# Kernel tuning notes

Hardware: AMD Instinct MI355X
Metric: run time of the kernel (lower is better)

## Reference

```python
import jax, jax.numpy as jnp
import numpy as np

TEMPERATURE = 2.0
ALPHA = 0.5
BETA = 0.5
EMB_SCALE = 0.02  # keep exp(scores) finite (original uses exp without max-subtraction)

N_TOKENS = 4096
VOCAB = 32000
DIM = 1024


def setup_inputs() -> dict:
    key = jax.random.key(0)
    k1, k2, k3, k4, k5 = jax.random.split(key, 5)
    batch = jax.random.randint(k1, (N_TOKENS,), 0, VOCAB)
    lang_emb = jax.random.normal(k2, (VOCAB, DIM), dtype=jnp.float32) * EMB_SCALE
    key_emb = jax.random.normal(k3, (VOCAB, DIM), dtype=jnp.float32) * EMB_SCALE
    value_emb = jax.random.normal(k4, (VOCAB, DIM), dtype=jnp.float32) * EMB_SCALE
    W = jax.random.normal(k5, (DIM, DIM), dtype=jnp.float32) * (1.0 / np.sqrt(DIM))
    b = jnp.zeros((DIM,), dtype=jnp.float32)
    return {"batch": batch, "lang_emb": lang_emb, "key_emb": key_emb,
            "value_emb": value_emb, "W": W, "b": b}


def reference(batch, lang_emb, key_emb, value_emb, W, b):
    # query: language-specific embedding lookup  [N, d]
    query = lang_emb[batch]
    # bilinear-transformed universal keys  [V, d]
    tkeys = key_emb @ W.T + b
    # scores = mm(tkeys, query^T).T  -> [N, V]
    scores = query @ tkeys.T
    # exp-normalize WITHOUT max subtraction, with temperature (as in original)
    w = jnp.exp(scores) / TEMPERATURE
    w = w / jnp.sum(w, axis=1, keepdims=True)
    # weighted universal value sum  [N, d]
    value = w @ value_emb
    # interpolate with direct value-embedding lookup
    return ALPHA * value_emb[batch] + BETA * value
```

## Files before the change

### kernel.cpp

```cpp
#include <hip/hip_runtime.h>


#define DIM   1024
#define VOCAB 32000
#define NTOK  4096

typedef unsigned short u16;
typedef unsigned char  u8;
typedef long long      i64t;
typedef __attribute__((ext_vector_type(2))) long long i64x2;
typedef __attribute__((ext_vector_type(8))) __bf16 bf16x8;
typedef __attribute__((ext_vector_type(4))) float  f32x4;
typedef __attribute__((ext_vector_type(8))) u16    u16x8;
typedef __attribute__((ext_vector_type(4))) u16    u16x4;
typedef __attribute__((ext_vector_type(8))) u8     u8x8;

__device__ __forceinline__ u16 f2bf(float f) {
  unsigned u = __float_as_uint(f);
  u += 0x7FFFu + ((u >> 16) & 1u);
  return (u16)(u >> 16);
}
__device__ __forceinline__ float bf2f(u16 s) {
  return __uint_as_float(((unsigned)s) << 16);
}
__device__ __forceinline__ u8 f2e4m3(float f) {
  unsigned u = __float_as_uint(f);
  unsigned s = (u >> 24) & 0x80u;
  int e = (int)((u >> 23) & 0xFF);
  unsigned m = u & 0x7FFFFF;
  int te = e - 127 + 7;
  if (te >= 1) {
    unsigned keep = m >> 20;
    unsigned rest = m & 0xFFFFF;
    keep += (rest > 0x80000u) || (rest == 0x80000u && (keep & 1));
    if (keep == 8) { keep = 0; te += 1; }
    return (u8)(s | ((unsigned)te << 3) | keep);
  } else {
    float q = fabsf(f) * 512.0f;
    int qi = (int)rintf(q);
    if (qi > 7) return (u8)(s | (1u << 3));
    return (u8)(s | (unsigned)qi);
  }
}
__device__ __forceinline__ u8 f2e4m3_exp(float e) {
  float sc = (e >= 1.0f) ? 8.0f : 16.0f;
  int   bo = (e >= 1.0f) ? 48 : 40;
  return (u8)(bo + (int)rintf(e * sc));
}
__device__ __forceinline__ int kperm(int k) {
  return ((k >> 3) & 3) * 16 + ((k >> 5) << 3) + (k & 7);
}

#define SB() __builtin_amdgcn_sched_barrier(0)
#define BAR() { SB(); __builtin_amdgcn_s_barrier(); SB(); }


__global__ void cvt_f32_bf16(const float* __restrict__ in, u16* __restrict__ out) {
  size_t i = (size_t)blockIdx.x * 256 + threadIdx.x;
  float4 v = ((const float4*)in)[i];
  u16x4 o; o[0]=f2bf(v.x); o[1]=f2bf(v.y); o[2]=f2bf(v.z); o[3]=f2bf(v.w);
  ((u16x4*)out)[i] = o;
}

__global__ void gather_q(const int* __restrict__ batch, const float* __restrict__ lang,
                         u16* __restrict__ q) {
  int row = blockIdx.x;
  int src = batch[row];
  int t = threadIdx.x;
  float4 v = *(const float4*)(lang + (size_t)src * DIM + (t << 2));
  u16x4 o; o[0]=f2bf(v.x); o[1]=f2bf(v.y); o[2]=f2bf(v.z); o[3]=f2bf(v.w);
  *(u16x4*)(q + (size_t)row * DIM + (t << 2)) = o;
}

__global__ void transpose_cvt(const float* __restrict__ in, u16* __restrict__ out,
                              int ldin, int ldout) {
  __shared__ u16 t[64][66];
  int r0 = blockIdx.x << 6;
  int c0 = blockIdx.y << 6;
  int tid = threadIdx.x;
  #pragma unroll
  for (int p = 0; p < 4; ++p) {
    int r = (p << 4) + (tid >> 4);
    int c = (tid & 15) << 2;
    float4 v = *(const float4*)(in + (size_t)(r0 + r) * ldin + c0 + c);
    t[c+0][r] = f2bf(v.x);
    t[c+1][r] = f2bf(v.y);
    t[c+2][r] = f2bf(v.z);
    t[c+3][r] = f2bf(v.w);
  }
  __syncthreads();
  #pragma unroll
  for (int qq = 0; qq < 2; ++qq) {
    int rr = tid >> 2;
    int cc = (((tid & 3) << 1) + qq) << 3;
    u16x8 w;
    #pragma unroll
    for (int j = 0; j < 8; ++j) w[j] = t[rr][cc + j];
    *(u16x8*)(out + (size_t)(c0 + rr) * ldout + r0 + cc) = w;
  }
}

__global__ void cvt_key_f8(const float* __restrict__ in, u8* __restrict__ out) {
  size_t g = (size_t)blockIdx.x * 256 + threadIdx.x;
  size_t row = g >> 7;
  int gg = (int)(g & 127);
  int b = gg >> 3, G = gg & 7;
  int O = ((G & 1) << 2) + (G >> 1);
  const float* src = in + row * DIM + (b << 6) + (O << 3);
  float4 v0 = *(const float4*)src;
  float4 v1 = *(const float4*)(src + 4);
  u8x8 o;
  o[0]=f2e4m3(16.f*v0.x); o[1]=f2e4m3(16.f*v0.y); o[2]=f2e4m3(16.f*v0.z); o[3]=f2e4m3(16.f*v0.w);
  o[4]=f2e4m3(16.f*v1.x); o[5]=f2e4m3(16.f*v1.y); o[6]=f2e4m3(16.f*v1.z); o[7]=f2e4m3(16.f*v1.w);
  *(u8x8*)(out + row * DIM + (b << 6) + (G << 3)) = o;
}

__global__ void cvt_qw_f8(const u16* __restrict__ in, u8* __restrict__ out) {
  size_t g = (size_t)blockIdx.x * 256 + threadIdx.x;
  size_t row = g >> 7;
  int gg = (int)(g & 127);
  int b = gg >> 3, G = gg & 7;
  int O = ((G & 1) << 2) + (G >> 1);
  u16x8 v = *(const u16x8*)(in + row * DIM + (b << 6) + (O << 3));
  u8x8 o;
  #pragma unroll
  for (int j = 0; j < 8; ++j) o[j] = f2e4m3(16.f * bf2f(v[j]));
  *(u8x8*)(out + row * DIM + (b << 6) + (G << 3)) = o;
}

__global__ void transpose_cvt_f8(const float* __restrict__ in, u8* __restrict__ out) {
  __shared__ float t[64][65];
  int r0 = blockIdx.x << 6;
  int c0 = blockIdx.y << 6;
  int tid = threadIdx.x;
  #pragma unroll
  for (int p = 0; p < 4; ++p) {
    int r = (p << 4) + (tid >> 4);
    int c = (tid & 15) << 2;
    float4 v = *(const float4*)(in + (size_t)(r0 + r) * DIM + c0 + c);
    t[c+0][r] = v.x; t[c+1][r] = v.y; t[c+2][r] = v.z; t[c+3][r] = v.w;
  }
  __syncthreads();
  #pragma unroll
  for (int qq = 0; qq < 2; ++qq) {
    int rr = tid >> 2;
    int O  = ((tid & 3) << 1) + qq;
    int cc = O << 3;
    int Gp = ((O & 3) << 1) + (O >> 2);
    u8x8 w;
    #pragma unroll
    for (int j = 0; j < 8; ++j) w[j] = f2e4m3(16.f * t[rr][cc + j]);
    *(u8x8*)(out + (size_t)(c0 + rr) * VOCAB + r0 + (Gp << 3)) = w;
  }
}

__global__ void gemm_qw(const u16* __restrict__ A, const u16* __restrict__ B,
                        u16* __restrict__ C, int K, int kSteps, int ldc) {
  __shared__ u16 As[128 * 32];
  __shared__ u16 Bs[128 * 32];
  const int tid  = threadIdx.x;
  const int lane = tid & 63;
  const int wid  = tid >> 6;
  const int wr   = wid >> 1, wc = wid & 1;
  const int row0 = blockIdx.x << 7;
  const int col0 = blockIdx.y << 7;

  f32x4 acc[4][4];
  #pragma unroll
  for (int m = 0; m < 4; ++m)
    #pragma unroll
    for (int n = 0; n < 4; ++n) acc[m][n] = (f32x4){0.f,0.f,0.f,0.f};

  const int sr = lane >> 2;
  const int sc = (lane & 3) << 3;

  for (int ks = 0; ks < kSteps; ++ks) {
    const int kk = ks << 5;
    #pragma unroll
    for (int t = 0; t < 2; ++t) {
      const int i = wid * 2 + t;
      const u16* gA = A + (size_t)(row0 + (i << 4) + sr) * K + kk + sc;
      const u16* gB = B + (size_t)(col0 + (i << 4) + sr) * K + kk + sc;
      __builtin_amdgcn_global_load_lds((const __attribute__((address_space(1))) void*)gA,
                                       (__attribute__((address_space(3))) void*)(As + i * 512),
                                       16, 0, 0);
      __builtin_amdgcn_global_load_lds((const __attribute__((address_space(1))) void*)gB,
                                       (__attribute__((address_space(3))) void*)(Bs + i * 512),
                                       16, 0, 0);
    }
    __syncthreads();
    bf16x8 a[4], b[4];
    #pragma unroll
    for (int m = 0; m < 4; ++m)
      a[m] = *(const bf16x8*)(As + ((wr << 6) + (m << 4) + (lane & 15)) * 32 + ((lane >> 4) << 3));
    #pragma unroll
    for (int n = 0; n < 4; ++n)
      b[n] = *(const bf16x8*)(Bs + ((wc << 6) + (n << 4) + (lane & 15)) * 32 + ((lane >> 4) << 3));
    #pragma unroll
    for (int m = 0; m < 4; ++m)
      #pragma unroll
      for (int n = 0; n < 4; ++n)
        acc[m][n] = __builtin_amdgcn_mfma_f32_16x16x32_bf16(a[m], b[n], acc[m][n], 0, 0, 0);
    __syncthreads();
  }

  const int r0 = row0 + (wr << 6);
  const int c0 = col0 + (wc << 6);
  const int fq = (lane >> 4) << 2;
  const int fr = lane & 15;
  #pragma unroll
  for (int m = 0; m < 4; ++m)
    #pragma unroll
    for (int n = 0; n < 4; ++n) {
      int col = c0 + (n << 4) + fr;
      #pragma unroll
      for (int j = 0; j < 4; ++j) {
        int row = r0 + (m << 4) + fq + j;
        C[(size_t)row * ldc + col] = f2bf(acc[m][n][j]);
      }
    }
}

#define STG8E(s, kk)                                                               \
  {                                                                                \
    _Pragma("unroll")                                                              \
    for (int c = 0; c < 4; ++c) {                                                  \
      const int ra = (c << 6) + (tid >> 3);                                        \
      const int ua = (tid & 7) ^ ((ra >> 1) & 7);                                  \
      const u8* gA = A + (size_t)(row0 + ra) * Kb + (kk) + (ua << 4);              \
      __builtin_amdgcn_global_load_lds(                                            \
          (const __attribute__((address_space(1))) void*)gA,                       \
          (__attribute__((address_space(3))) void*)(lds + (s) * 65536 + (c << 13) + tid * 16), \
          16, 0, 0);                                                               \
    }                                                                              \
    _Pragma("unroll")                                                              \
    for (int c = 0; c < 4; ++c) {                                                  \
      const int rn = (c << 6) + (tid >> 3);                                        \
      const int un = (tid & 7) ^ ((rn >> 1) & 7);                                  \
      const u8* gB = B + (size_t)(col0 + rn) * Kb + (kk) + (un << 4);              \
      __builtin_amdgcn_global_load_lds(                                            \
          (const __attribute__((address_space(1))) void*)gB,                       \
          (__attribute__((address_space(3))) void*)(lds + (s) * 65536 + 32768 + (c << 13) + tid * 16), \
          16, 0, 0);                                                               \
    }                                                                              \
  }

#define KTILE128(t, NT)                                                            \
  {                                                                                \
    SB(); asm volatile("s_waitcnt vmcnt(0)"); SB();                                \
    BAR();                                                                         \
    if ((t) + 1 < (NT)) STG8E(((t) + 1) & 1, (((t) + 1) << 7) + kb0)               \
    const u8* Ab = lds + ((t) & 1) * 65536;                                        \
    const u8* Bb = Ab + 32768;                                                     \
    _Pragma("unroll")                                                              \
    for (int nh = 0; nh < 2; ++nh)                                                 \
      _Pragma("unroll")                                                            \
      for (int nq = 0; nq < 2; ++nq) {                                             \
        const int row = (wc << 6) + (nh << 5) + (nq << 4) + fr;                    \
        const int sw  = (row >> 1) & 7;                                            \
        i64x2 v0 = *(const i64x2*)(Bb + row * 128 + ((fq ^ sw) << 4));             \
        b0[nh][nq][0] = v0[0]; b0[nh][nq][1] = v0[1];                              \
        i64x2 v1 = *(const i64x2*)(Bb + row * 128 + (((4 + fq) ^ sw) << 4));       \
        b1[nh][nq][0] = v1[0]; b1[nh][nq][1] = v1[1];                              \
      }                                                                            \
    _Pragma("unroll")                                                              \
    for (int mq = 0; mq < 8; ++mq) {                                               \
      const int row = (wr << 7) + ((mq >> 2) << 6) + ((mq & 3) << 4) + fr;         \
      const int sw  = (row >> 1) & 7;                                              \
      i64x2 v0 = *(const i64x2*)(Ab + row * 128 + ((fq ^ sw) << 4));               \
      a0[mq][0] = v0[0]; a0[mq][1] = v0[1];                                        \
      i64x2 v1 = *(const i64x2*)(Ab + row * 128 + (((4 + fq) ^ sw) << 4));         \
      a1[mq][0] = v1[0]; a1[mq][1] = v1[1];                                        \
    }                                                                              \
    __builtin_amdgcn_s_setprio(1);                                                 \
    _Pragma("unroll")                                                              \
    for (int m = 0; m < 8; ++m)                                                    \
      _Pragma("unroll")                                                            \
      for (int nh = 0; nh < 2; ++nh)                                               \
        _Pragma("unroll")                                                          \
        for (int nq = 0; nq < 2; ++nq)                                             \
          _Pragma("unroll")                                                        \
          for (int ks = 0; ks < 2; ++ks)                                           \
            acc[m][(nh << 1) + nq] = __builtin_amdgcn_mfma_f32_16x16x32_fp8_fp8(   \
                a0[m][ks], b0[nh][nq][ks], acc[m][(nh << 1) + nq], 0, 0, 0);       \
    _Pragma("unroll")                                                              \
    for (int m = 0; m < 8; ++m)                                                    \
      _Pragma("unroll")                                                            \
      for (int nh = 0; nh < 2; ++nh)                                               \
        _Pragma("unroll")                                                          \
        for (int nq = 0; nq < 2; ++nq)                                             \
          _Pragma("unroll")                                                        \
          for (int ks = 0; ks < 2; ++ks)                                           \
            acc[m][(nh << 1) + nq] = __builtin_amdgcn_mfma_f32_16x16x32_fp8_fp8(   \
                a1[m][ks], b1[nh][nq][ks], acc[m][(nh << 1) + nq], 0, 0, 0);       \
    __builtin_amdgcn_s_setprio(0);                                                 \
  }

__global__ __launch_bounds__(512, 1) void gemm256e8(const u8* __restrict__ A,
                                                    const u8* __restrict__ B,
                                                    u8* __restrict__ P,
                                                    float* __restrict__ dpart,
                                                    int Kb, int nTiles) {
  __shared__ __align__(16) u8 lds[131072];
  const int tid  = threadIdx.x;
  const int lane = tid & 63;
  const int wid  = tid >> 6;
  const int wr   = wid >> 2;
  const int wc   = wid & 3;

  const int nwg = (int)(gridDim.x * gridDim.y);
  int lin = blockIdx.y * gridDim.x + blockIdx.x;
  { const int cpx = nwg >> 3; lin = (lin & 7) * cpx + (lin >> 3); }
  const int row0 = (lin & 15) << 8;
  const int cblk = lin >> 4;
  const int col0 = cblk << 8;
  const int kb0 = 0;

  const int fr = lane & 15;
  const int fq = lane >> 4;

  f32x4 acc[8][4];
  #pragma unroll
  for (int m = 0; m < 8; ++m)
    #pragma unroll
    for (int n = 0; n < 4; ++n) acc[m][n] = (f32x4){0.f, 0.f, 0.f, 0.f};

  i64t a0[8][2], a1[8][2], b0[2][2][2], b1[2][2][2];

  STG8E(0, kb0)
  for (int t = 0; t < nTiles; ++t) KTILE128(t, nTiles)

  const float inv256 = 1.0f / 256.0f;
  float rs[32];
  #pragma unroll
  for (int i = 0; i < 32; ++i) rs[i] = 0.f;
  #pragma unroll
  for (int m = 0; m < 8; ++m)
    #pragma unroll
    for (int n = 0; n < 4; ++n) {
      const int l6  = (n << 4) + fr;
      const int col = col0 + (wc << 6) + kperm(l6);
      #pragma unroll
      for (int j = 0; j < 4; ++j) {
        const int row = row0 + (wr << 7) + (m << 4) + (fq << 2) + j;
        float e = __expf(acc[m][n][j] * inv256);
        P[(size_t)row * VOCAB + col] = f2e4m3_exp(e);
        rs[(m << 2) + j] += e;
      }
    }
  #pragma unroll
  for (int i = 0; i < 32; ++i) {
    #pragma unroll
    for (int s = 8; s >= 1; s >>= 1) rs[i] += __shfl_xor(rs[i], s, 16);
  }
  __syncthreads();
  float* dsm = (float*)lds;
  if (fr == 0) {
    #pragma unroll
    for (int m = 0; m < 8; ++m)
      #pragma unroll
      for (int j = 0; j < 4; ++j)
        dsm[(wc << 8) + (wr << 7) + (m << 4) + (fq << 2) + j] = rs[(m << 2) + j];
  }
  __syncthreads();
  if (tid < 256)
    dpart[(size_t)(row0 + tid) * 256 + cblk] =
        dsm[tid] + dsm[256 + tid] + dsm[512 + tid] + dsm[768 + tid];
}

__global__ __launch_bounds__(512, 1) void gemm256p8(const u8* __restrict__ A,
                                                    const u8* __restrict__ B,
                                                    float* __restrict__ Cout,
                                                    int Kb) {
  __shared__ __align__(16) u8 lds[131072];
  const int tid  = threadIdx.x;
  const int lane = tid & 63;
  const int wid  = tid >> 6;
  const int wr   = wid >> 2;
  const int wc   = wid & 3;

  const int nwg = (int)(gridDim.x * gridDim.y);
  int lin = blockIdx.y * gridDim.x + blockIdx.x;
  { const int cpx = nwg >> 3; lin = (lin & 7) * cpx + (lin >> 3); }
  const int row0 = (lin & 15) << 8;
  const int col0 = (lin >> 4) << 8;

  const int z = blockIdx.z;
  const int nT = (z < 2) ? 32 : 31;
  const int kb0 = ((z < 2) ? (z * 32) : (64 + (z - 2) * 31)) << 7;

  const int fr = lane & 15;
  const int fq = lane >> 4;

  f32x4 acc[8][4];
  #pragma unroll
  for (int m = 0; m < 8; ++m)
    #pragma unroll
    for (int n = 0; n < 4; ++n) acc[m][n] = (f32x4){0.f, 0.f, 0.f, 0.f};

  i64t a0[8][2], a1[8][2], b0[2][2][2], b1[2][2][2];

  STG8E(0, kb0)
  for (int t = 0; t < nT; ++t) KTILE128(t, nT)

  float* C = Cout + (size_t)z * NTOK * DIM;
  #pragma unroll
  for (int m = 0; m < 8; ++m)
    #pragma unroll
    for (int n = 0; n < 4; ++n) {
      const int col = col0 + (wc << 6) + (n << 4) + fr;
      #pragma unroll
      for (int j = 0; j < 4; ++j) {
        const int row = row0 + (wr << 7) + (m << 4) + (fq << 2) + j;
        C[(size_t)row * DIM + col] = acc[m][n][j];
      }
    }
}

__global__ __launch_bounds__(256, 2) void gemm128e(const u16* __restrict__ A,
                                                   const u16* __restrict__ B,
                                                   u16* __restrict__ P,
                                                   float* __restrict__ dpart,
                                                   int K, int nTiles, int ldc, int cb0) {
  __shared__ __align__(16) u16 lds[32768];
  const int tid  = threadIdx.x;
  const int lane = tid & 63;
  const int wid  = tid >> 6;
  const int wr   = wid >> 1;
  const int wc   = wid & 1;

  const int nwg = (int)(gridDim.x * gridDim.y);
  int lin = blockIdx.y * gridDim.x + blockIdx.x;
  { const int cpx = nwg >> 3; lin = (lin & 7) * cpx + (lin >> 3); }
  const int row0 = (lin & 31) << 7;
  const int cblk = lin >> 5;
  const int col0 = cblk << 7;

  const int fr = lane & 15;
  const int fq = lane >> 4;
  const int rb = tid >> 3;
  const int ss = tid & 7;

#define STG128(d, kk)                                                              \
  {                                                                                \
    _Pragma("unroll")                                                              \
    for (int c = 0; c < 4; ++c) {                                                  \
      const int ra = (c << 5) + rb;                                                \
      const u16* gA = A + (size_t)(row0 + ra) * K + (kk) + ((ss ^ (ra & 7)) << 3); \
      __builtin_amdgcn_global_load_lds(                                            \
          (const __attribute__((address_space(1))) void*)gA,                       \
          (__attribute__((address_space(3))) void*)(lds + (d) * 16384 + (((c << 5) + (wid << 3)) << 6)), \
          16, 0, 0);                                                               \
    }                                                                              \
    _Pragma("unroll")                                                              \
    for (int c = 0; c < 4; ++c) {                                                  \
      const int rn = (c << 5) + rb;                                                \
      const u16* gB = B + (size_t)(col0 + rn) * K + (kk) + ((ss ^ (rn & 7)) << 3); \
      __builtin_amdgcn_global_load_lds(                                            \
          (const __attribute__((address_space(1))) void*)gB,                       \
          (__attribute__((address_space(3))) void*)(lds + (d) * 16384 + 8192 + (((c << 5) + (wid << 3)) << 6)), \
          16, 0, 0);                                                               \
    }                                                                              \
  }

  f32x4 acc[4][4];
  #pragma unroll
  for (int m = 0; m < 4; ++m)
    #pragma unroll
    for (int n = 0; n < 4; ++n) acc[m][n] = (f32x4){0.f, 0.f, 0.f, 0.f};

  STG128(0, 0)
  STG128(1, 64)

  bf16x8 a[4], b[4];

  for (int t = 0; t < nTiles; ++t) {
    const int d = t & 1;
    const u16* Abuf = lds + d * 16384;
    const u16* Bbuf = Abuf + 8192;
    SB();
    if (t + 1 < nTiles) { asm volatile("s_waitcnt vmcnt(8)"); }
    else                { asm volatile("s_waitcnt vmcnt(0)"); }
    BAR();

    #pragma unroll
    for (int ks = 0; ks < 2; ++ks) {
      #pragma unroll
      for (int mq = 0; mq < 4; ++mq) {
        const int row  = (wr << 6) + (mq << 4) + fr;
        const int slot = ((ks << 2) + fq) ^ (row & 7);
        a[mq] = *(const bf16x8*)(Abuf + (row << 6) + (slot << 3));
      }
      #pragma unroll
      for (int nq = 0; nq < 4; ++nq) {
        const int row  = (wc << 6) + (nq << 4) + fr;
        const int slot = ((ks << 2) + fq) ^ (row & 7);
        b[nq] = *(const bf16x8*)(Bbuf + (row << 6) + (slot << 3));
      }
      __builtin_amdgcn_s_setprio(1);
      #pragma unroll
      for (int mq = 0; mq < 4; ++mq)
        #pragma unroll
        for (int nq = 0; nq < 4; ++nq)
          acc[mq][nq] = __builtin_amdgcn_mfma_f32_16x16x32_bf16(
              a[mq], b[nq], acc[mq][nq], 0, 0, 0);
      __builtin_amdgcn_s_setprio(0);
    }
    BAR();
    if (t + 2 < nTiles) STG128(d, (t + 2) << 6)
  }
#undef STG128

  float rs[16];
  #pragma unroll
  for (int i = 0; i < 16; ++i) rs[i] = 0.f;
  #pragma unroll
  for (int mq = 0; mq < 4; ++mq)
    #pragma unroll
    for (int nq = 0; nq < 4; ++nq) {
      const int col = col0 + (wc << 6) + (nq << 4) + fr;
      #pragma unroll
      for (int j = 0; j < 4; ++j) {
        const int row = row0 + (wr << 6) + (mq << 4) + (fq << 2) + j;
        float e = __expf(acc[mq][nq][j]);
        P[(size_t)row * ldc + col] = f2bf(e);
        rs[(mq << 2) + j] += e;
      }
    }
  #pragma unroll
  for (int i = 0; i < 16; ++i) {
    #pragma unroll
    for (int s = 8; s >= 1; s >>= 1) rs[i] += __shfl_xor(rs[i], s, 16);
  }
  __syncthreads();
  float* dsm = (float*)lds;
  if (fr == 0) {
    #pragma unroll
    for (int mq = 0; mq < 4; ++mq)
      #pragma unroll
      for (int j = 0; j < 4; ++j)
        dsm[(wc << 7) + (wr << 6) + (mq << 4) + (fq << 2) + j] = rs[(mq << 2) + j];
  }
  __syncthreads();
  if (tid < 128)
    dpart[(size_t)(row0 + tid) * 256 + cb0 + cblk] = dsm[tid] + dsm[128 + tid];
}

#define STG256(d, kk)                                                              \
  {                                                                                \
    _Pragma("unroll")                                                              \
    for (int c = 0; c < 4; ++c) {                                                  \
      const int ra = (c << 6) + rb;                                                \
      const u16* gA = A + (size_t)(row0 + ra) * K + (kk) + ((ss ^ (ra & 7)) << 3); \
      __builtin_amdgcn_global_load_lds(                                            \
          (const __attribute__((address_space(1))) void*)gA,                       \
          (__attribute__((address_space(3))) void*)(lds + (d) * 32768 + (((c << 6) + (wid << 3)) << 6)), \
          16, 0, 0);                                                               \
    }                                                                              \
    _Pragma("unroll")                                                              \
    for (int c = 0; c < 4; ++c) {                                                  \
      const int rn = (c << 6) + rb;                                                \
      const u16* gB = B + (size_t)(col0 + rn) * K + (kk) + ((ss ^ (rn & 7)) << 3); \
      __builtin_amdgcn_global_load_lds(                                            \
          (const __attribute__((address_space(1))) void*)gB,                       \
          (__attribute__((address_space(3))) void*)(lds + (d) * 32768 + 16384 + (((c << 6) + (wid << 3)) << 6)), \
          16, 0, 0);                                                               \
    }                                                                              \
  }

__global__ __launch_bounds__(512, 2) void gemm256acc(const u16* __restrict__ A,
                                                     const u16* __restrict__ B,
                                                     float* __restrict__ Cout,
                                                     int K, int nTiles, int ldc) {
  __shared__ __align__(16) u16 lds[65536];
  const int tid  = threadIdx.x;
  const int lane = tid & 63;
  const int wid  = tid >> 6;
  const int wr   = wid >> 2;
  const int wc   = wid & 3;

  const int nwg = (int)(gridDim.x * gridDim.y);
  int lin = blockIdx.y * gridDim.x + blockIdx.x;
  { const int cpx = nwg >> 3; lin = (lin & 7) * cpx + (lin >> 3); }
  const int row0 = (lin & 15) << 8;
  const int col0 = (lin >> 4) << 8;

  const int kbase = blockIdx.z * (nTiles << 6);
  const int fr = lane & 15;
  const int fq = lane >> 4;
  const int rb = tid >> 3;
  const int ss = tid & 7;

  f32x4 acc[8][4];
  #pragma unroll
  for (int m = 0; m < 8; ++m)
    #pragma unroll
    for (int n = 0; n < 4; ++n) acc[m][n] = (f32x4){0.f, 0.f, 0.f, 0.f};

  bf16x8 a[4][2], b[2][2][2];

  STG256(0, kbase)
  STG256(1, kbase + 64)
  for (int t = 0; t < nTiles; ++t) {
    const int d = t & 1;
    const u16* Abuf = lds + d * 32768;
    const u16* Bbuf = Abuf + 16384;
    SB();
    if (t + 1 < nTiles) { asm volatile("s_waitcnt vmcnt(8)"); }
    else                { asm volatile("s_waitcnt vmcnt(0)"); }
    BAR();
    #pragma unroll
    for (int nh = 0; nh < 2; ++nh)
      #pragma unroll
      for (int nq = 0; nq < 2; ++nq)
        #pragma unroll
        for (int ks = 0; ks < 2; ++ks) {
          const int row  = (wc << 6) + (nh << 5) + (nq << 4) + fr;
          const int slot = ((ks << 2) + fq) ^ (row & 7);
          b[nh][nq][ks] = *(const bf16x8*)(Bbuf + (row << 6) + (slot << 3));
        }
    #pragma unroll
    for (int mh = 0; mh < 2; ++mh) {
      #pragma unroll
      for (int mq = 0; mq < 4; ++mq)
        #pragma unroll
        for (int ks = 0; ks < 2; ++ks) {
          const int row  = (wr << 7) + (mh << 6) + (mq << 4) + fr;
          const int slot = ((ks << 2) + fq) ^ (row & 7);
          a[mq][ks] = *(const bf16x8*)(Abuf + (row << 6) + (slot << 3));
        }
      __builtin_amdgcn_s_setprio(1);
      #pragma unroll
      for (int mq = 0; mq < 4; ++mq)
        #pragma unroll
        for (int nh = 0; nh < 2; ++nh)
          #pragma unroll
          for (int nq = 0; nq < 2; ++nq)
            #pragma unroll
            for (int ks = 0; ks < 2; ++ks)
              acc[(mh << 2) + mq][(nh << 1) + nq] =
                  __builtin_amdgcn_mfma_f32_16x16x32_bf16(
                      a[mq][ks], b[nh][nq][ks], acc[(mh << 2) + mq][(nh << 1) + nq], 0, 0, 0);
      __builtin_amdgcn_s_setprio(0);
    }
    BAR();
    if (t + 2 < nTiles) STG256(d, kbase + ((t + 2) << 6))
  }

  float* C = Cout + (size_t)blockIdx.z * NTOK * DIM;
  #pragma unroll
  for (int m = 0; m < 8; ++m)
    #pragma unroll
    for (int n = 0; n < 4; ++n) {
      const int col = col0 + (wc << 6) + (n << 4) + fr;
      #pragma unroll
      for (int j = 0; j < 4; ++j) {
        const int row = row0 + (wr << 7) + (m << 4) + (fq << 2) + j;
        C[(size_t)row * ldc + col] += acc[m][n][j];
      }
    }
}

__global__ void denom_reduce(const float* __restrict__ dpart, float* __restrict__ denom,
                             int npart) {
  int row = blockIdx.x;
  int l = threadIdx.x;
  float s = 0.f;
  #pragma unroll
  for (int k = 0; k < 4; ++k) {
    int idx = l + (k << 6);
    if (idx < npart) s += dpart[(size_t)row * 256 + idx];
  }
  #pragma unroll
  for (int off = 32; off >= 1; off >>= 1) s += __shfl_down(s, off, 64);
  if (l == 0) denom[row] = s;
}

__global__ void finalize(const float* __restrict__ parts, const float* __restrict__ denom,
                         const float* __restrict__ ve, const int* __restrict__ batch,
                         float* __restrict__ out, int nks, float pvInv) {
  int row = blockIdx.x;
  int t = threadIdx.x;
  float inv = 0.5f * pvInv / denom[row];
  float4 a = *(const float4*)(ve + (size_t)batch[row] * DIM + (t << 2));
  float sx = 0.f, sy = 0.f, sz = 0.f, sw = 0.f;
  for (int ks = 0; ks < nks; ++ks) {
    float4 pv = *(const float4*)(parts + ((size_t)ks * NTOK + row) * DIM + (t << 2));
    sx += pv.x; sy += pv.y; sz += pv.z; sw += pv.w;
  }
  float4 o;
  o.x = 0.5f * a.x + inv * sx;
  o.y = 0.5f * a.y + inv * sy;
  o.z = 0.5f * a.z + inv * sz;
  o.w = 0.5f * a.w + inv * sw;
  *(float4*)(out + (size_t)row * DIM + (t << 2)) = o;
}

extern "C" void kernel_launch(void* const* d_in, const int* in_sizes, int n_in,
                              void* d_out, int out_size, void* d_ws, size_t ws_size,
                              hipStream_t stream) {
  const int*   batch = (const int*)d_in[0];
  const float* lang  = (const float*)d_in[1];
  const float* key   = (const float*)d_in[2];
  const float* ve    = (const float*)d_in[3];
  const float* W     = (const float*)d_in[4];
  float* out = (float*)d_out;

  const size_t szWt    = (size_t)DIM * DIM * 2;
  const size_t szQb    = (size_t)NTOK * DIM * 2;
  const size_t szQW    = (size_t)NTOK * DIM * 2;
  const size_t szDpart = (size_t)NTOK * 256 * 4;
  const size_t szDenom = (size_t)NTOK * 4;
  const size_t base    = szWt + szQb + szQW + szDpart + szDenom;

  char* ws = (char*)d_ws;
  u16*   Wt    = (u16*)(ws);
  u16*   qb    = (u16*)(ws + szWt);
  u16*   qW    = (u16*)(ws + szWt + szQb);
  float* dpart = (float*)(ws + szWt + szQb + szQW);
  float* denom = (float*)(ws + szWt + szQb + szQW + szDpart);

  const int KSF = 8;
  const size_t szPartsF = (size_t)KSF * NTOK * DIM * 4;
  const size_t szQW8    = (size_t)NTOK * DIM;
  const size_t szKey8   = (size_t)VOCAB * DIM;
  const size_t szVeT8   = (size_t)DIM * VOCAB;
  const size_t szP8     = (size_t)NTOK * VOCAB;
  const bool fullP = (base + szPartsF + szQW8 + szKey8 + szVeT8 + szP8) <= ws_size;

  transpose_cvt<<<dim3(DIM / 64, DIM / 64), 256, 0, stream>>>(W, Wt, DIM, DIM);
  gather_q<<<NTOK, 256, 0, stream>>>(batch, lang, qb);
  gemm_qw<<<dim3(NTOK / 128, DIM / 128), 256, 0, stream>>>(qb, Wt, qW, DIM, DIM / 32, DIM);

  if (fullP) {
    float* parts = (float*)(ws + base);
    u8*    qW8   = (u8*)(ws + base + szPartsF);
    u8*    key8  = (u8*)(ws + base + szPartsF + szQW8);
    u8*    veT8  = (u8*)(ws + base + szPartsF + szQW8 + szKey8);
    u8*    P8    = (u8*)(ws + base + szPartsF + szQW8 + szKey8 + szVeT8);

    cvt_qw_f8<<<NTOK * DIM / 8 / 256, 256, 0, stream>>>(qW, qW8);
    cvt_key_f8<<<VOCAB * DIM / 8 / 256, 256, 0, stream>>>(key, key8);
    transpose_cvt_f8<<<dim3(VOCAB / 64, DIM / 64), 256, 0, stream>>>(ve, veT8);

    gemm256e8<<<dim3(NTOK / 256, VOCAB / 256), 512, 0, stream>>>(qW8, key8, P8, dpart,
                                                                 DIM, DIM / 128);
    denom_reduce<<<NTOK, 64, 0, stream>>>(dpart, denom, VOCAB / 256);
    gemm256p8<<<dim3(NTOK / 256, DIM / 256, KSF), 512, 0, stream>>>(P8, veT8, parts, VOCAB);
    finalize<<<NTOK, 256, 0, stream>>>(parts, denom, ve, batch, out, KSF, 1.0f / 16.0f);
  } else {
    const int KS = 2;
    const size_t szParts = (size_t)KS * NTOK * DIM * 4;
    int CHUNK = 1280;
    {
      const int copt[2] = {6400, 1280};
      for (int i = 0; i < 2; ++i) {
        size_t need = base + szParts + (size_t)copt[i] * (NTOK * 2 + DIM * 4);
        if (need <= ws_size) { CHUNK = copt[i]; break; }
      }
    }
    const int NCHUNK = VOCAB / CHUNK;
    float* parts = (float*)(ws + base);
    char*  dyn   = ws + base + szParts;
    u16*   keyc  = (u16*)(dyn);
    u16*   veTc  = (u16*)(dyn + (size_t)CHUNK * DIM * 2);
    u16*   Pc    = (u16*)(dyn + (size_t)CHUNK * DIM * 4);

    hipMemsetAsync(parts, 0, szParts, stream);
    for (int c = 0; c < NCHUNK; ++c) {
      const int v0 = c * CHUNK;
      cvt_f32_bf16<<<CHUNK * DIM / 1024, 256, 0, stream>>>(key + (size_t)v0 * DIM, keyc);
      transpose_cvt<<<dim3(CHUNK / 64, DIM / 64), 256, 0, stream>>>(ve + (size_t)v0 * DIM, veTc,
                                                                    DIM, CHUNK);
      gemm128e<<<dim3(NTOK / 128, CHUNK / 128), 256, 0, stream>>>(qW, keyc, Pc, dpart,
                                                                  DIM, DIM / 64, CHUNK, v0 >> 7);
      gemm256acc<<<dim3(NTOK / 256, DIM / 256, KS), 512, 0, stream>>>(Pc, veTc, parts,
                                                                      CHUNK, CHUNK / 64 / KS, DIM);
    }
    denom_reduce<<<NTOK, 64, 0, stream>>>(dpart, denom, 250);
    finalize<<<NTOK, 256, 0, stream>>>(parts, denom, ve, batch, out, KS, 1.0f);
  }
}
```

Measured before the change: 539.6 us.

## Use scaled 16x16x128 FP8 MFMA and drop K-permutation layouts

Replaces the pairs of 16x16x32 fp8 MFMAs in both FP8 GEMMs with the single gfx950 scaled MFMA (16x16x128 f8f6f4), loading 32-byte contiguous fragments per lane. The scale arguments fold the 1/256 and 1/16 factors into the instruction. The k-permuted layouts in the conversion kernels and the kperm column remap in the exp epilogue go away. This cuts MFMA instruction count and fragment shuffling, at the cost of wider register fragments and an assumption that the scale encodings are correct.

```diff
diff --git a/kernel.cpp b/kernel.cpp
--- a/kernel.cpp
+++ b/kernel.cpp
@@ -7,13 +7,13 @@
 
 typedef unsigned short u16;
 typedef unsigned char  u8;
-typedef long long      i64t;
-typedef __attribute__((ext_vector_type(2))) long long i64x2;
 typedef __attribute__((ext_vector_type(8))) __bf16 bf16x8;
 typedef __attribute__((ext_vector_type(4))) float  f32x4;
 typedef __attribute__((ext_vector_type(8))) u16    u16x8;
 typedef __attribute__((ext_vector_type(4))) u16    u16x4;
 typedef __attribute__((ext_vector_type(8))) u8     u8x8;
+typedef __attribute__((ext_vector_type(4))) int    i32x4;
+typedef __attribute__((ext_vector_type(8))) int    i32x8;
 
 __device__ __forceinline__ u16 f2bf(float f) {
   unsigned u = __float_as_uint(f);
@@ -47,9 +47,6 @@
   int   bo = (e >= 1.0f) ? 48 : 40;
   return (u8)(bo + (int)rintf(e * sc));
 }
-__device__ __forceinline__ int kperm(int k) {
-  return ((k >> 3) & 3) * 16 + ((k >> 5) << 3) + (k & 7);
-}
 
 #define SB() __builtin_amdgcn_sched_barrier(0)
 #define BAR() { SB(); __builtin_amdgcn_s_barrier(); SB(); }
@@ -100,32 +97,24 @@
   }
 }
 
-__global__ void cvt_key_f8(const float* __restrict__ in, u8* __restrict__ out) {
+__global__ void cvt_f32_f8(const float* __restrict__ in, u8* __restrict__ out) {
   size_t g = (size_t)blockIdx.x * 256 + threadIdx.x;
-  size_t row = g >> 7;
-  int gg = (int)(g & 127);
-  int b = gg >> 3, G = gg & 7;
-  int O = ((G & 1) << 2) + (G >> 1);
-  const float* src = in + row * DIM + (b << 6) + (O << 3);
+  const float* src = in + g * 8;
   float4 v0 = *(const float4*)src;
   float4 v1 = *(const float4*)(src + 4);
   u8x8 o;
   o[0]=f2e4m3(16.f*v0.x); o[1]=f2e4m3(16.f*v0.y); o[2]=f2e4m3(16.f*v0.z); o[3]=f2e4m3(16.f*v0.w);
   o[4]=f2e4m3(16.f*v1.x); o[5]=f2e4m3(16.f*v1.y); o[6]=f2e4m3(16.f*v1.z); o[7]=f2e4m3(16.f*v1.w);
-  *(u8x8*)(out + row * DIM + (b << 6) + (G << 3)) = o;
+  *(u8x8*)(out + g * 8) = o;
 }
 
 __global__ void cvt_qw_f8(const u16* __restrict__ in, u8* __restrict__ out) {
   size_t g = (size_t)blockIdx.x * 256 + threadIdx.x;
-  size_t row = g >> 7;
-  int gg = (int)(g & 127);
-  int b = gg >> 3, G = gg & 7;
-  int O = ((G & 1) << 2) + (G >> 1);
-  u16x8 v = *(const u16x8*)(in + row * DIM + (b << 6) + (O << 3));
+  u16x8 v = *(const u16x8*)(in + g * 8);
   u8x8 o;
   #pragma unroll
   for (int j = 0; j < 8; ++j) o[j] = f2e4m3(16.f * bf2f(v[j]));
-  *(u8x8*)(out + row * DIM + (b << 6) + (G << 3)) = o;
+  *(u8x8*)(out + g * 8) = o;
 }
 
 __global__ void transpose_cvt_f8(const float* __restrict__ in, u8* __restrict__ out) {
@@ -144,13 +133,11 @@
   #pragma unroll
   for (int qq = 0; qq < 2; ++qq) {
     int rr = tid >> 2;
-    int O  = ((tid & 3) << 1) + qq;
-    int cc = O << 3;
-    int Gp = ((O & 3) << 1) + (O >> 2);
+    int cc = (((tid & 3) << 1) + qq) << 3;
     u8x8 w;
     #pragma unroll
     for (int j = 0; j < 8; ++j) w[j] = f2e4m3(16.f * t[rr][cc + j]);
-    *(u8x8*)(out + (size_t)(c0 + rr) * VOCAB + r0 + (Gp << 3)) = w;
+    *(u8x8*)(out + (size_t)(c0 + rr) * VOCAB + r0 + cc) = w;
   }
 }
 
@@ -245,54 +232,39 @@
     }                                                                              \
   }
 
-#define KTILE128(t, NT)                                                            \
+#define KTILE128S(t, NT, SCA, SCB)                                                 \
   {                                                                                \
     SB(); asm volatile("s_waitcnt vmcnt(0)"); SB();                                \
     BAR();                                                                         \
     if ((t) + 1 < (NT)) STG8E(((t) + 1) & 1, (((t) + 1) << 7) + kb0)               \
     const u8* Ab = lds + ((t) & 1) * 65536;                                        \
     const u8* Bb = Ab + 32768;                                                     \
-    _Pragma("unroll")                                                              \
-    for (int nh = 0; nh < 2; ++nh)                                                 \
+    i32x8 aF[8], bF[4];                                                            \
+    _Pragma("unroll")                                                              \
+    for (int n = 0; n < 4; ++n) {                                                  \
+      const int row = (wc << 6) + (n << 4) + fr;                                   \
+      const int sw  = (row >> 1) & 7;                                              \
+      i32x4 lo = *(const i32x4*)(Bb + row * 128 + ((((fq << 1) + 0) ^ sw) << 4));  \
+      i32x4 hi = *(const i32x4*)(Bb + row * 128 + ((((fq << 1) + 1) ^ sw) << 4));  \
       _Pragma("unroll")                                                            \
-      for (int nq = 0; nq < 2; ++nq) {                                             \
-        const int row = (wc << 6) + (nh << 5) + (nq << 4) + fr;                    \
-        const int sw  = (row >> 1) & 7;                                            \
-        i64x2 v0 = *(const i64x2*)(Bb + row * 128 + ((fq ^ sw) << 4));             \
-        b0[nh][nq][0] = v0[0]; b0[nh][nq][1] = v0[1];                              \
-        i64x2 v1 = *(const i64x2*)(Bb + row * 128 + (((4 + fq) ^ sw) << 4));       \
-        b1[nh][nq][0] = v1[0]; b1[nh][nq][1] = v1[1];                              \
-      }                                                                            \
-    _Pragma("unroll")                                                              \
-    for (int mq = 0; mq < 8; ++mq) {                                               \
-      const int row = (wr << 7) + ((mq >> 2) << 6) + ((mq & 3) << 4) + fr;         \
+      for (int j = 0; j < 4; ++j) { bF[n][j] = lo[j]; bF[n][4 + j] = hi[j]; }      \
+    }                                                                              \
+    _Pragma("unroll")                                                              \
+    for (int m = 0; m < 8; ++m) {                                                  \
+      const int row = (wr << 7) + (m << 4) + fr;                                   \
       const int sw  = (row >> 1) & 7;                                              \
-      i64x2 v0 = *(const i64x2*)(Ab + row * 128 + ((fq ^ sw) << 4));               \
-      a0[mq][0] = v0[0]; a0[mq][1] = v0[1];                                        \
-      i64x2 v1 = *(const i64x2*)(Ab + row * 128 + (((4 + fq) ^ sw) << 4));         \
-      a1[mq][0] = v1[0]; a1[mq][1] = v1[1];                                        \
+      i32x4 lo = *(const i32x4*)(Ab + row * 128 + ((((fq << 1) + 0) ^ sw) << 4));  \
+      i32x4 hi = *(const i32x4*)(Ab + row * 128 + ((((fq << 1) + 1) ^ sw) << 4));  \
+      _Pragma("unroll")                                                            \
+      for (int j = 0; j < 4; ++j) { aF[m][j] = lo[j]; aF[m][4 + j] = hi[j]; }      \
     }                                                                              \
     __builtin_amdgcn_s_setprio(1);                                                 \
     _Pragma("unroll")                                                              \
     for (int m = 0; m < 8; ++m)                                                    \
       _Pragma("unroll")                                                            \
-      for (int nh = 0; nh < 2; ++nh)                                               \
-        _Pragma("unroll")                                                          \
-        for (int nq = 0; nq < 2; ++nq)                                             \
-          _Pragma("unroll")                                                        \
-          for (int ks = 0; ks < 2; ++ks)                                           \
-            acc[m][(nh << 1) + nq] = __builtin_amdgcn_mfma_f32_16x16x32_fp8_fp8(   \
-                a0[m][ks], b0[nh][nq][ks], acc[m][(nh << 1) + nq], 0, 0, 0);       \
-    _Pragma("unroll")                                                              \
-    for (int m = 0; m < 8; ++m)                                                    \
-      _Pragma("unroll")                                                            \
-      for (int nh = 0; nh < 2; ++nh)                                               \
-        _Pragma("unroll")                                                          \
-        for (int nq = 0; nq < 2; ++nq)                                             \
-          _Pragma("unroll")                                                        \
-          for (int ks = 0; ks < 2; ++ks)                                           \
-            acc[m][(nh << 1) + nq] = __builtin_amdgcn_mfma_f32_16x16x32_fp8_fp8(   \
-                a1[m][ks], b1[nh][nq][ks], acc[m][(nh << 1) + nq], 0, 0, 0);       \
+      for (int n = 0; n < 4; ++n)                                                  \
+        acc[m][n] = __builtin_amdgcn_mfma_scale_f32_16x16x128_f8f6f4(              \
+            aF[m], bF[n], acc[m][n], 0, 0, 0, (SCA), 0, (SCB));                    \
     __builtin_amdgcn_s_setprio(0);                                                 \
   }
 
@@ -325,12 +297,9 @@
     #pragma unroll
     for (int n = 0; n < 4; ++n) acc[m][n] = (f32x4){0.f, 0.f, 0.f, 0.f};
 
-  i64t a0[8][2], a1[8][2], b0[2][2][2], b1[2][2][2];
-
   STG8E(0, kb0)
-  for (int t = 0; t < nTiles; ++t) KTILE128(t, nTiles)
-
-  const float inv256 = 1.0f / 256.0f;
+  for (int t = 0; t < nTiles; ++t) KTILE128S(t, nTiles, 123, 123)
+
   float rs[32];
   #pragma unroll
   for (int i = 0; i < 32; ++i) rs[i] = 0.f;
@@ -338,12 +307,11 @@
   for (int m = 0; m < 8; ++m)
     #pragma unroll
     for (int n = 0; n < 4; ++n) {
-      const int l6  = (n << 4) + fr;
-      const int col = col0 + (wc << 6) + kperm(l6);
+      const int col = col0 + (wc << 6) + (n << 4) + fr;
       #pragma unroll
       for (int j = 0; j < 4; ++j) {
         const int row = row0 + (wr << 7) + (m << 4) + (fq << 2) + j;
-        float e = __expf(acc[m][n][j] * inv256);
+        float e = __expf(acc[m][n][j]);
         P[(size_t)row * VOCAB + col] = f2e4m3_exp(e);
         rs[(m << 2) + j] += e;
       }
@@ -398,10 +366,8 @@
     #pragma unroll
     for (int n = 0; n < 4; ++n) acc[m][n] = (f32x4){0.f, 0.f, 0.f, 0.f};
 
-  i64t a0[8][2], a1[8][2], b0[2][2][2], b1[2][2][2];
-
   STG8E(0, kb0)
-  for (int t = 0; t < nT; ++t) KTILE128(t, nT)
+  for (int t = 0; t < nT; ++t) KTILE128S(t, nT, 127, 127)
 
   float* C = Cout + (size_t)z * NTOK * DIM;
   #pragma unroll
@@ -740,7 +706,7 @@
     u8*    P8    = (u8*)(ws + base + szPartsF + szQW8 + szKey8 + szVeT8);
 
     cvt_qw_f8<<<NTOK * DIM / 8 / 256, 256, 0, stream>>>(qW, qW8);
-    cvt_key_f8<<<VOCAB * DIM / 8 / 256, 256, 0, stream>>>(key, key8);
+    cvt_f32_f8<<<VOCAB * DIM / 8 / 256, 256, 0, stream>>>(key, key8);
     transpose_cvt_f8<<<dim3(VOCAB / 64, DIM / 64), 256, 0, stream>>>(ve, veT8);
 
     gemm256e8<<<dim3(NTOK / 256, VOCAB / 256), 512, 0, stream>>>(qW8, key8, P8, dpart,
```

Result: faster. 472.8 us (-12.4%).
